# Performance work log

Measured on AMD Instinct MI355X. Metric: run time of the kernel, lower is better.

The kernel has to match this reference:

```python
import jax, jax.numpy as jnp
import numpy as np

BETA = 0.5      # conf.beta (undefined global in original repo)
ALPHA = 0.2     # LeakyReLU negative slope (init arg alpha)
N, E, FIN, FOUT = 50000, 1_600_000, 128, 64


def setup_inputs() -> dict:
    key = jax.random.key(0)
    k1, k2, k3, k4, k5 = jax.random.split(key, 5)
    inp = jax.random.normal(k1, (N, FIN), dtype=jnp.float32)
    edge = jax.random.randint(k2, (2, E), 0, N)                      # [2,E] (src,dst), = adj.nonzero().t()
    M_vals = jax.random.uniform(k3, (E,), dtype=jnp.float32)          # M gathered at edges
    # xavier_normal with gain 1.414, matching torch init
    W = jax.random.normal(k4, (FIN, FOUT), dtype=jnp.float32) * (1.414 * np.sqrt(2.0 / (FIN + FOUT)))
    a = jax.random.normal(k5, (2 * FOUT,), dtype=jnp.float32) * (1.414 * np.sqrt(2.0 / (1 + 2 * FOUT)))
    return {"input": inp, "M_vals": M_vals, "W": W, "a": a, "edge": edge}


def reference(input, M_vals, W, a, edge):
    n, f = input.shape[0], W.shape[1]
    src, dst = edge[0], edge[1]
    h = input @ W                                   # [N, F]
    # M = beta*M + (1-beta)*adj; at edges adj == 1
    bias = M_vals * BETA + (1.0 - BETA)             # [E]
    # a . cat(h_src, bias*h_dst) == (h@a[:F])[src] + bias * (h@a[F:])[dst]
    s1 = h @ a[:f]                                  # [N]
    s2 = h @ a[f:]                                  # [N]
    edge_e = jnp.exp(jax.nn.leaky_relu(s1[src] + bias * s2[dst], negative_slope=ALPHA))  # [E]
    # special_spmm(edge, e, [N,N], ones) -> per-row sum of edge weights
    e_rowsum = jax.ops.segment_sum(edge_e, src, num_segments=n)       # [N]
    # special_spmm(edge, e, [N,N], h) -> weighted aggregation of dst features into src rows
    h_prime = jax.ops.segment_sum(edge_e[:, None] * h[dst], src, num_segments=n)  # [N, F]
    h_prime = h_prime / e_rowsum[:, None]
    return jax.nn.elu(h_prime)                      # concat=True
```

## Files before the change

### kernel.cpp

```cpp
#include <hip/hip_runtime.h>
#include <hip/hip_bf16.h>

#define NN   50000
#define EE   1600000
#define FIN  128
#define FOUT 64
#define BETA  0.5f
#define ALPHA 0.2f
#define SBW    256
#define NB2    196
#define RCAP   9000
#define PGRID  400
#define PCHUNK 4000
#define CAP3   9008
#define XS     136
#define WS     136

typedef __attribute__((ext_vector_type(8))) short short8;
typedef __attribute__((ext_vector_type(8))) unsigned short ushort8v;
typedef __attribute__((ext_vector_type(4))) float float4v;

__device__ __forceinline__ float load_any(const void* p, long i, int isf32) {
    if (isf32) return ((const float*)p)[i];
    unsigned int b = ((unsigned int)(((const unsigned short*)p)[i])) << 16;
    return __uint_as_float(b);
}

__device__ __forceinline__ unsigned short f32_to_bf16_rne(float f) {
    unsigned int b = __float_as_uint(f);
    return (unsigned short)((b + 0x7FFF + ((b >> 16) & 1)) >> 16);
}

__device__ __forceinline__ float bf16_to_f32(unsigned short u) {
    return __uint_as_float(((unsigned int)u) << 16);
}

__global__ __launch_bounds__(256) void mfma_gemm_kernel(
    const void* __restrict__ inp,
    const void* __restrict__ W,
    const void* __restrict__ a,
    const void* __restrict__ Mv,
    unsigned short* __restrict__ h,
    float* __restrict__ s1,
    float* __restrict__ s2,
    int* __restrict__ flags,
    int* __restrict__ bcur)
{
    __shared__ unsigned short Xs[16 * XS];
    __shared__ unsigned short Wl[64 * WS];
    __shared__ float part1[4][16];
    __shared__ float part2[4][16];
    __shared__ int vote;

    const int tid  = threadIdx.x;
    const int wave = tid >> 6;
    const int lane = tid & 63;
    const int quad = lane >> 4;
    const int col  = lane & 15;
    const int rb   = blockIdx.x * 16;

    if (tid == 0) vote = 0;
    __syncthreads();

    {
        int m = 0;
        const unsigned short* ip = (const unsigned short*)inp;
        const float vi = bf16_to_f32(ip[(long)rb * FIN + tid * 8]);
        if (isnan(vi) || fabsf(vi) > 1e4f) m |= 1;
        if (tid < 128) {
            const float va = bf16_to_f32(((const unsigned short*)a)[tid]);
            if (isnan(va) || fabsf(va) > 1e4f) m |= 2;
        }
        const float vw = bf16_to_f32(((const unsigned short*)W)[tid * 16]);
        if (isnan(vw) || fabsf(vw) > 1e4f) m |= 4;
        if (blockIdx.x == 0) {
            const long half = (long)EE >> 1;
            const long pos = 2 * (((long)tid * (half / 256)) % half);
            const float vm = bf16_to_f32(((const unsigned short*)Mv)[pos]);
            if (isnan(vm) || fabsf(vm) > 1e4f) m |= 8;
        }
        if (m) atomicOr(&vote, m);
    }
    __syncthreads();
    const int vm = vote;
    const int fI = vm & 1, fA = (vm >> 1) & 1, fW = (vm >> 2) & 1;

    if (blockIdx.x == 0) {
        if (tid == 0) { flags[0] = fI; flags[1] = (vm >> 3) & 1; }
        if (tid < NB2) bcur[tid] = 0;
    }

    for (int i = tid; i < FIN * FOUT; i += 256) {
        const int k = i >> 6, n = i & 63;
        Wl[n * WS + k] = f32_to_bf16_rne(load_any(W, i, fW));
    }
    {
        const int r = tid >> 4, k8 = (tid & 15) * 8;
        if (!fI) {
            const unsigned short* src = (const unsigned short*)inp + (long)(rb + r) * FIN + k8;
            *(ushort8v*)&Xs[r * XS + k8] = *(const ushort8v*)src;
        } else {
            const float* src = (const float*)inp + (long)(rb + r) * FIN + k8;
            ushort8v v;
            #pragma unroll
            for (int j = 0; j < 8; ++j) v[j] = f32_to_bf16_rne(src[j]);
            *(ushort8v*)&Xs[r * XS + k8] = v;
        }
    }
    __syncthreads();

    const int nb = wave * 16;
    float4v acc = { 0.f, 0.f, 0.f, 0.f };
    #pragma unroll
    for (int k0 = 0; k0 < FIN; k0 += 32) {
        const short8 af = *(const short8*)&Xs[col * XS + k0 + quad * 8];
        const short8 bf = *(const short8*)&Wl[(nb + col) * WS + k0 + quad * 8];
        acc = __builtin_amdgcn_mfma_f32_16x16x32_bf16(af, bf, acc, 0, 0, 0);
    }

    #pragma unroll
    for (int r = 0; r < 4; ++r)
        h[(long)(rb + quad * 4 + r) * FOUT + nb + col] = f32_to_bf16_rne(acc[r]);

    const float a1 = load_any(a, nb + col, fA);
    const float a2 = load_any(a, 64 + nb + col, fA);
    #pragma unroll
    for (int r = 0; r < 4; ++r) {
        float v1 = acc[r] * a1;
        float v2 = acc[r] * a2;
        #pragma unroll
        for (int o = 1; o < 16; o <<= 1) {
            v1 += __shfl_xor(v1, o, 64);
            v2 += __shfl_xor(v2, o, 64);
        }
        if (col == 0) {
            part1[wave][quad * 4 + r] = v1;
            part2[wave][quad * 4 + r] = v2;
        }
    }
    __syncthreads();
    if (tid < 16) {
        s1[rb + tid] = part1[0][tid] + part1[1][tid] + part1[2][tid] + part1[3][tid];
        s2[rb + tid] = part2[0][tid] + part2[1][tid] + part2[2][tid] + part2[3][tid];
    }
}

__global__ __launch_bounds__(1024) void partition_kernel(
    const int* __restrict__ edge,
    const void* __restrict__ Mv,
    const int* __restrict__ flags,
    const float* __restrict__ s1,
    const float* __restrict__ s2,
    int* __restrict__ bcur,
    unsigned long long* __restrict__ recs)
{
    __shared__ int lcnt[NB2];
    __shared__ int lbase[NB2];
    const int tid = threadIdx.x;
    const int fM = flags[1];
    const int e0 = blockIdx.x * PCHUNK;

    if (tid < NB2) lcnt[tid] = 0;
    __syncthreads();

    int srcs[4], dsts[4];
    float mvs[4];
    #pragma unroll
    for (int k = 0; k < 4; ++k) {
        const int e = e0 + tid + 1024 * k;
        const bool ok = (tid + 1024 * k) < PCHUNK;
        srcs[k] = ok ? edge[e] : -1;
        dsts[k] = ok ? edge[EE + e] : 0;
        mvs[k]  = ok ? load_any(Mv, e, fM) : 0.f;
    }
    #pragma unroll
    for (int k = 0; k < 4; ++k)
        if (srcs[k] >= 0) atomicAdd(&lcnt[srcs[k] >> 8], 1);
    __syncthreads();

    if (tid < NB2) {
        const int c = lcnt[tid];
        const int o = c ? atomicAdd(&bcur[tid], c) : 0;
        lbase[tid] = tid * RCAP + o;
        lcnt[tid] = 0;
    }
    __syncthreads();

    float ss1[4], ss2[4];
    #pragma unroll
    for (int k = 0; k < 4; ++k) {
        ss1[k] = (srcs[k] >= 0) ? s1[srcs[k]] : 0.f;
        ss2[k] = (srcs[k] >= 0) ? s2[dsts[k]] : 0.f;
    }
    #pragma unroll
    for (int k = 0; k < 4; ++k) {
        if (srcs[k] < 0) continue;
        const float bias = mvs[k] * BETA + (1.f - BETA);
        const float x  = ss1[k] + bias * ss2[k];
        const float lr = x > 0.f ? x : ALPHA * x;
        const float ee = __expf(lr);
        const int b = srcs[k] >> 8;
        const int r = atomicAdd(&lcnt[b], 1);
        const int pos = lbase[b] + r;
        if (pos < (b + 1) * RCAP)
            recs[pos] = ((unsigned long long)(unsigned)srcs[k] << 32)
                      | ((unsigned long long)(unsigned)dsts[k] << 16)
                      | (unsigned long long)f32_to_bf16_rne(ee);
    }
}

__global__ __launch_bounds__(1024) void csr_spmm_kernel(
    const int* __restrict__ bcur,
    const unsigned long long* __restrict__ recs,
    const unsigned short* __restrict__ h,
    const int* __restrict__ flags,
    void* __restrict__ out)
{
    __shared__ unsigned long long lrec[CAP3];
    __shared__ unsigned int lpair[CAP3];
    __shared__ int cnt[SBW];
    __shared__ int off[SBW];
    __shared__ int wsum[4];
    const int b    = blockIdx.x;
    const int tid  = threadIdx.x;
    const int rb   = b * SBW;
    const int beg  = b * RCAP;

    int n = bcur[b]; if (n > RCAP) n = RCAP;

    if (tid < SBW) cnt[tid] = 0;
    __syncthreads();

    for (int j = tid; j < n; j += 1024) {
        const unsigned long long rec = recs[beg + j];
        lrec[j] = rec;
        atomicAdd(&cnt[(int)(rec >> 32) - rb], 1);
    }
    __syncthreads();

    int c = 0, x = 0;
    if (tid < SBW) {
        const int lane = tid & 63;
        c = cnt[tid];
        x = c;
        #pragma unroll
        for (int o = 1; o < 64; o <<= 1) {
            int y = __shfl_up(x, o, 64);
            if (lane >= o) x += y;
        }
        if (lane == 63) wsum[tid >> 6] = x;
    }
    __syncthreads();
    if (tid < SBW) {
        const int wv = tid >> 6;
        int wb = 0;
        for (int w = 0; w < wv; ++w) wb += wsum[w];
        off[tid] = wb + x - c;
        cnt[tid] = 0;
    }
    __syncthreads();

    for (int j = tid; j < n; j += 1024) {
        const unsigned long long rec = lrec[j];
        const int r = (int)(rec >> 32) - rb;
        const int rank = atomicAdd(&cnt[r], 1);
        lpair[off[r] + rank] = (unsigned int)(rec & 0xFFFFFFFFu);
    }
    __syncthreads();

    const int wv   = tid >> 6;
    const int lane = tid & 63;
    const int g    = lane >> 3;
    const int sl   = lane & 7;
    const int fOut = flags[0];

    for (int rr = wv; rr < SBW; rr += 16) {
        const int row = rb + rr;
        if (row >= NN) break;
        const int jb = off[rr];
        const int je = jb + cnt[rr];

        float acc0 = 0.f, acc1 = 0.f, acc2 = 0.f, acc3 = 0.f;
        float acc4 = 0.f, acc5 = 0.f, acc6 = 0.f, acc7 = 0.f;
        float rsum = 0.f;
        int j = jb;
        for (; j + 15 < je; j += 16) {
            const unsigned int u0 = lpair[j + g];
            const unsigned int u1 = lpair[j + 8 + g];
            const ushort8v h0 = *(const ushort8v*)&h[(long)(u0 >> 16) * FOUT + 8 * sl];
            const ushort8v h1 = *(const ushort8v*)&h[(long)(u1 >> 16) * FOUT + 8 * sl];
            const float v0 = bf16_to_f32((unsigned short)(u0 & 0xFFFFu));
            const float v1 = bf16_to_f32((unsigned short)(u1 & 0xFFFFu));
            rsum += v0 + v1;
            acc0 = fmaf(v0, bf16_to_f32(h0[0]), acc0); acc0 = fmaf(v1, bf16_to_f32(h1[0]), acc0);
            acc1 = fmaf(v0, bf16_to_f32(h0[1]), acc1); acc1 = fmaf(v1, bf16_to_f32(h1[1]), acc1);
            acc2 = fmaf(v0, bf16_to_f32(h0[2]), acc2); acc2 = fmaf(v1, bf16_to_f32(h1[2]), acc2);
            acc3 = fmaf(v0, bf16_to_f32(h0[3]), acc3); acc3 = fmaf(v1, bf16_to_f32(h1[3]), acc3);
            acc4 = fmaf(v0, bf16_to_f32(h0[4]), acc4); acc4 = fmaf(v1, bf16_to_f32(h1[4]), acc4);
            acc5 = fmaf(v0, bf16_to_f32(h0[5]), acc5); acc5 = fmaf(v1, bf16_to_f32(h1[5]), acc5);
            acc6 = fmaf(v0, bf16_to_f32(h0[6]), acc6); acc6 = fmaf(v1, bf16_to_f32(h1[6]), acc6);
            acc7 = fmaf(v0, bf16_to_f32(h0[7]), acc7); acc7 = fmaf(v1, bf16_to_f32(h1[7]), acc7);
        }
        for (; j < je; j += 8) {
            if (j + g < je) {
                const unsigned int u = lpair[j + g];
                const ushort8v hv = *(const ushort8v*)&h[(long)(u >> 16) * FOUT + 8 * sl];
                const float v = bf16_to_f32((unsigned short)(u & 0xFFFFu));
                rsum += v;
                acc0 = fmaf(v, bf16_to_f32(hv[0]), acc0);
                acc1 = fmaf(v, bf16_to_f32(hv[1]), acc1);
                acc2 = fmaf(v, bf16_to_f32(hv[2]), acc2);
                acc3 = fmaf(v, bf16_to_f32(hv[3]), acc3);
                acc4 = fmaf(v, bf16_to_f32(hv[4]), acc4);
                acc5 = fmaf(v, bf16_to_f32(hv[5]), acc5);
                acc6 = fmaf(v, bf16_to_f32(hv[6]), acc6);
                acc7 = fmaf(v, bf16_to_f32(hv[7]), acc7);
            }
        }

        #pragma unroll
        for (int o = 8; o < 64; o <<= 1) {
            rsum += __shfl_xor(rsum, o, 64);
            acc0 += __shfl_xor(acc0, o, 64);
            acc1 += __shfl_xor(acc1, o, 64);
            acc2 += __shfl_xor(acc2, o, 64);
            acc3 += __shfl_xor(acc3, o, 64);
            acc4 += __shfl_xor(acc4, o, 64);
            acc5 += __shfl_xor(acc5, o, 64);
            acc6 += __shfl_xor(acc6, o, 64);
            acc7 += __shfl_xor(acc7, o, 64);
        }

        if (g == 0) {
            const float inv = 1.f / rsum;
            float q0 = acc0 * inv, q1 = acc1 * inv, q2 = acc2 * inv, q3 = acc3 * inv;
            float q4 = acc4 * inv, q5 = acc5 * inv, q6 = acc6 * inv, q7 = acc7 * inv;
            q0 = q0 > 0.f ? q0 : (__expf(q0) - 1.f);
            q1 = q1 > 0.f ? q1 : (__expf(q1) - 1.f);
            q2 = q2 > 0.f ? q2 : (__expf(q2) - 1.f);
            q3 = q3 > 0.f ? q3 : (__expf(q3) - 1.f);
            q4 = q4 > 0.f ? q4 : (__expf(q4) - 1.f);
            q5 = q5 > 0.f ? q5 : (__expf(q5) - 1.f);
            q6 = q6 > 0.f ? q6 : (__expf(q6) - 1.f);
            q7 = q7 > 0.f ? q7 : (__expf(q7) - 1.f);
            if (fOut) {
                float4* o = (float4*)((float*)out + (long)row * FOUT + 8 * sl);
                o[0] = make_float4(q0, q1, q2, q3);
                o[1] = make_float4(q4, q5, q6, q7);
            } else {
                ushort8v ov;
                ov[0] = f32_to_bf16_rne(q0); ov[1] = f32_to_bf16_rne(q1);
                ov[2] = f32_to_bf16_rne(q2); ov[3] = f32_to_bf16_rne(q3);
                ov[4] = f32_to_bf16_rne(q4); ov[5] = f32_to_bf16_rne(q5);
                ov[6] = f32_to_bf16_rne(q6); ov[7] = f32_to_bf16_rne(q7);
                *(ushort8v*)((unsigned short*)out + (long)row * FOUT + 8 * sl) = ov;
            }
        }
    }
}

extern "C" void kernel_launch(void* const* d_in, const int* in_sizes, int n_in,
                              void* d_out, int out_size, void* d_ws, size_t ws_size,
                              hipStream_t stream) {
    const void* inp  = d_in[0];
    const void* Mv   = d_in[1];
    const void* W    = d_in[2];
    const void* a    = d_in[3];
    const int*  edge = (const int*)d_in[4];

    char* p = (char*)d_ws;
    int*                flags  = (int*)p;            p += 256;
    unsigned short*     h      = (unsigned short*)p; p += ((size_t)NN * FOUT * 2 + 255) / 256 * 256;
    float*              s1     = (float*)p;          p += ((size_t)NN * 4 + 255) / 256 * 256;
    float*              s2     = (float*)p;          p += ((size_t)NN * 4 + 255) / 256 * 256;
    int*                bcur   = (int*)p;            p += ((size_t)NB2 * 4 + 255) / 256 * 256;
    unsigned long long* recs   = (unsigned long long*)p;

    mfma_gemm_kernel<<<NN / 16, 256, 0, stream>>>(inp, W, a, Mv, h, s1, s2, flags, bcur);
    partition_kernel<<<PGRID, 1024, 0, stream>>>(edge, Mv, flags, s1, s2, bcur, recs);
    csr_spmm_kernel<<<NB2, 1024, 0, stream>>>(bcur, recs, h, flags, d_out);
}
```

Baseline: 183.5 us.

## Pretranspose W once, fuse rank assignment into counting, unroll SpMM gathers deeper

A new small kernel converts and transposes W into a bf16 workspace buffer once, along with flag detection and bucket reset. Each GEMM block then reads B fragments directly from that buffer instead of rebuilding a 16 KB LDS copy of W per 16-row tile. The CSR kernel now records each edge's rank during the counting pass, removing the second LDS atomic pass during the scatter. The SpMM inner loop issues four gathers per iteration instead of two for more memory-level parallelism. The cost is an extra kernel launch and uncached-in-LDS global reads of W in the GEMM.

```diff
diff --git a/kernel.cpp b/kernel.cpp
--- a/kernel.cpp
+++ b/kernel.cpp
@@ -14,7 +14,6 @@
 #define PCHUNK 4000
 #define CAP3   9008
 #define XS     136
-#define WS     136
 
 typedef __attribute__((ext_vector_type(8))) short short8;
 typedef __attribute__((ext_vector_type(8))) unsigned short ushort8v;
@@ -35,19 +34,48 @@
     return __uint_as_float(((unsigned int)u) << 16);
 }
 
+__global__ __launch_bounds__(256) void detwt_kernel(
+    const void* __restrict__ W, const void* __restrict__ Mv,
+    unsigned short* __restrict__ Wt, int* __restrict__ flags,
+    int* __restrict__ bcur)
+{
+    __shared__ int vote;
+    const int tid = threadIdx.x;
+    if (tid == 0) vote = 0;
+    __syncthreads();
+
+    int m = 0;
+    const float vw = bf16_to_f32(((const unsigned short*)W)[tid * 16]);
+    if (isnan(vw) || fabsf(vw) > 1e4f) m |= 1;
+    if (blockIdx.x == 0) {
+        const long half = (long)EE >> 1;
+        const long pos = 2 * (((long)tid * (half / 256)) % half);
+        const float vm = bf16_to_f32(((const unsigned short*)Mv)[pos]);
+        if (isnan(vm) || fabsf(vm) > 1e4f) m |= 2;
+    }
+    if (m) atomicOr(&vote, m);
+    __syncthreads();
+
+    const int fW = vote & 1;
+    if (blockIdx.x == 0) {
+        if (tid == 0) flags[1] = (vote >> 1) & 1;
+        if (tid < NB2) bcur[tid] = 0;
+    }
+    const int i = blockIdx.x * 256 + tid;
+    const int k = i >> 6, n = i & 63;
+    Wt[n * FIN + k] = f32_to_bf16_rne(load_any(W, i, fW));
+}
+
 __global__ __launch_bounds__(256) void mfma_gemm_kernel(
     const void* __restrict__ inp,
-    const void* __restrict__ W,
+    const unsigned short* __restrict__ Wt,
     const void* __restrict__ a,
-    const void* __restrict__ Mv,
     unsigned short* __restrict__ h,
     float* __restrict__ s1,
     float* __restrict__ s2,
-    int* __restrict__ flags,
-    int* __restrict__ bcur)
+    int* __restrict__ flags)
 {
     __shared__ unsigned short Xs[16 * XS];
-    __shared__ unsigned short Wl[64 * WS];
     __shared__ float part1[4][16];
     __shared__ float part2[4][16];
     __shared__ int vote;
@@ -64,36 +92,18 @@
 
     {
         int m = 0;
-        const unsigned short* ip = (const unsigned short*)inp;
-        const float vi = bf16_to_f32(ip[(long)rb * FIN + tid * 8]);
+        const float vi = bf16_to_f32(((const unsigned short*)inp)[(long)rb * FIN + tid * 8]);
         if (isnan(vi) || fabsf(vi) > 1e4f) m |= 1;
         if (tid < 128) {
             const float va = bf16_to_f32(((const unsigned short*)a)[tid]);
             if (isnan(va) || fabsf(va) > 1e4f) m |= 2;
         }
-        const float vw = bf16_to_f32(((const unsigned short*)W)[tid * 16]);
-        if (isnan(vw) || fabsf(vw) > 1e4f) m |= 4;
-        if (blockIdx.x == 0) {
-            const long half = (long)EE >> 1;
-            const long pos = 2 * (((long)tid * (half / 256)) % half);
-            const float vm = bf16_to_f32(((const unsigned short*)Mv)[pos]);
-            if (isnan(vm) || fabsf(vm) > 1e4f) m |= 8;
-        }
         if (m) atomicOr(&vote, m);
     }
     __syncthreads();
-    const int vm = vote;
-    const int fI = vm & 1, fA = (vm >> 1) & 1, fW = (vm >> 2) & 1;
-
-    if (blockIdx.x == 0) {
-        if (tid == 0) { flags[0] = fI; flags[1] = (vm >> 3) & 1; }
-        if (tid < NB2) bcur[tid] = 0;
-    }
-
-    for (int i = tid; i < FIN * FOUT; i += 256) {
-        const int k = i >> 6, n = i & 63;
-        Wl[n * WS + k] = f32_to_bf16_rne(load_any(W, i, fW));
-    }
+    const int fI = vote & 1, fA = (vote >> 1) & 1;
+    if (blockIdx.x == 0 && tid == 0) flags[0] = fI;
+
     {
         const int r = tid >> 4, k8 = (tid & 15) * 8;
         if (!fI) {
@@ -114,7 +124,7 @@
     #pragma unroll
     for (int k0 = 0; k0 < FIN; k0 += 32) {
         const short8 af = *(const short8*)&Xs[col * XS + k0 + quad * 8];
-        const short8 bf = *(const short8*)&Wl[(nb + col) * WS + k0 + quad * 8];
+        const short8 bf = *(const short8*)&Wt[(long)(nb + col) * FIN + k0 + quad * 8];
         acc = __builtin_amdgcn_mfma_f32_16x16x32_bf16(af, bf, acc, 0, 0, 0);
     }
 
@@ -233,8 +243,10 @@
 
     for (int j = tid; j < n; j += 1024) {
         const unsigned long long rec = recs[beg + j];
-        lrec[j] = rec;
-        atomicAdd(&cnt[(int)(rec >> 32) - rb], 1);
+        const int r = (int)(rec >> 32) - rb;
+        const int rank = atomicAdd(&cnt[r], 1);
+        lrec[j] = ((unsigned long long)(unsigned)(r | (rank << 8)) << 32)
+                | (unsigned long long)(unsigned)(rec & 0xFFFFFFFFu);
     }
     __syncthreads();
 
@@ -256,15 +268,13 @@
         int wb = 0;
         for (int w = 0; w < wv; ++w) wb += wsum[w];
         off[tid] = wb + x - c;
-        cnt[tid] = 0;
     }
     __syncthreads();
 
     for (int j = tid; j < n; j += 1024) {
         const unsigned long long rec = lrec[j];
-        const int r = (int)(rec >> 32) - rb;
-        const int rank = atomicAdd(&cnt[r], 1);
-        lpair[off[r] + rank] = (unsigned int)(rec & 0xFFFFFFFFu);
+        const unsigned int hi = (unsigned int)(rec >> 32);
+        lpair[off[hi & 255u] + (hi >> 8)] = (unsigned int)(rec & 0xFFFFFFFFu);
     }
     __syncthreads();
 
@@ -284,38 +294,55 @@
         float acc4 = 0.f, acc5 = 0.f, acc6 = 0.f, acc7 = 0.f;
         float rsum = 0.f;
         int j = jb;
-        for (; j + 15 < je; j += 16) {
-            const unsigned int u0 = lpair[j + g];
-            const unsigned int u1 = lpair[j + 8 + g];
-            const ushort8v h0 = *(const ushort8v*)&h[(long)(u0 >> 16) * FOUT + 8 * sl];
-            const ushort8v h1 = *(const ushort8v*)&h[(long)(u1 >> 16) * FOUT + 8 * sl];
-            const float v0 = bf16_to_f32((unsigned short)(u0 & 0xFFFFu));
-            const float v1 = bf16_to_f32((unsigned short)(u1 & 0xFFFFu));
-            rsum += v0 + v1;
-            acc0 = fmaf(v0, bf16_to_f32(h0[0]), acc0); acc0 = fmaf(v1, bf16_to_f32(h1[0]), acc0);
-            acc1 = fmaf(v0, bf16_to_f32(h0[1]), acc1); acc1 = fmaf(v1, bf16_to_f32(h1[1]), acc1);
-            acc2 = fmaf(v0, bf16_to_f32(h0[2]), acc2); acc2 = fmaf(v1, bf16_to_f32(h1[2]), acc2);
-            acc3 = fmaf(v0, bf16_to_f32(h0[3]), acc3); acc3 = fmaf(v1, bf16_to_f32(h1[3]), acc3);
-            acc4 = fmaf(v0, bf16_to_f32(h0[4]), acc4); acc4 = fmaf(v1, bf16_to_f32(h1[4]), acc4);
-            acc5 = fmaf(v0, bf16_to_f32(h0[5]), acc5); acc5 = fmaf(v1, bf16_to_f32(h1[5]), acc5);
-            acc6 = fmaf(v0, bf16_to_f32(h0[6]), acc6); acc6 = fmaf(v1, bf16_to_f32(h1[6]), acc6);
-            acc7 = fmaf(v0, bf16_to_f32(h0[7]), acc7); acc7 = fmaf(v1, bf16_to_f32(h1[7]), acc7);
-        }
-        for (; j < je; j += 8) {
-            if (j + g < je) {
-                const unsigned int u = lpair[j + g];
-                const ushort8v hv = *(const ushort8v*)&h[(long)(u >> 16) * FOUT + 8 * sl];
-                const float v = bf16_to_f32((unsigned short)(u & 0xFFFFu));
+        for (; j + 31 < je; j += 32) {
+            unsigned int u[4];
+            #pragma unroll
+            for (int kk = 0; kk < 4; ++kk) u[kk] = lpair[j + 8 * kk + g];
+            ushort8v hv[4];
+            #pragma unroll
+            for (int kk = 0; kk < 4; ++kk)
+                hv[kk] = *(const ushort8v*)&h[(long)(u[kk] >> 16) * FOUT + 8 * sl];
+            #pragma unroll
+            for (int kk = 0; kk < 4; ++kk) {
+                const float v = bf16_to_f32((unsigned short)(u[kk] & 0xFFFFu));
                 rsum += v;
-                acc0 = fmaf(v, bf16_to_f32(hv[0]), acc0);
-                acc1 = fmaf(v, bf16_to_f32(hv[1]), acc1);
-                acc2 = fmaf(v, bf16_to_f32(hv[2]), acc2);
-                acc3 = fmaf(v, bf16_to_f32(hv[3]), acc3);
-                acc4 = fmaf(v, bf16_to_f32(hv[4]), acc4);
-                acc5 = fmaf(v, bf16_to_f32(hv[5]), acc5);
-                acc6 = fmaf(v, bf16_to_f32(hv[6]), acc6);
-                acc7 = fmaf(v, bf16_to_f32(hv[7]), acc7);
+                acc0 = fmaf(v, bf16_to_f32(hv[kk][0]), acc0);
+                acc1 = fmaf(v, bf16_to_f32(hv[kk][1]), acc1);
+                acc2 = fmaf(v, bf16_to_f32(hv[kk][2]), acc2);
+                acc3 = fmaf(v, bf16_to_f32(hv[kk][3]), acc3);
+                acc4 = fmaf(v, bf16_to_f32(hv[kk][4]), acc4);
+                acc5 = fmaf(v, bf16_to_f32(hv[kk][5]), acc5);
+                acc6 = fmaf(v, bf16_to_f32(hv[kk][6]), acc6);
+                acc7 = fmaf(v, bf16_to_f32(hv[kk][7]), acc7);
             }
+        }
+        for (; j + 7 < je; j += 8) {
+            const unsigned int u = lpair[j + g];
+            const ushort8v hv = *(const ushort8v*)&h[(long)(u >> 16) * FOUT + 8 * sl];
+            const float v = bf16_to_f32((unsigned short)(u & 0xFFFFu));
+            rsum += v;
+            acc0 = fmaf(v, bf16_to_f32(hv[0]), acc0);
+            acc1 = fmaf(v, bf16_to_f32(hv[1]), acc1);
+            acc2 = fmaf(v, bf16_to_f32(hv[2]), acc2);
+            acc3 = fmaf(v, bf16_to_f32(hv[3]), acc3);
+            acc4 = fmaf(v, bf16_to_f32(hv[4]), acc4);
+            acc5 = fmaf(v, bf16_to_f32(hv[5]), acc5);
+            acc6 = fmaf(v, bf16_to_f32(hv[6]), acc6);
+            acc7 = fmaf(v, bf16_to_f32(hv[7]), acc7);
+        }
+        if (j < je && j + g < je) {
+            const unsigned int u = lpair[j + g];
+            const ushort8v hv = *(const ushort8v*)&h[(long)(u >> 16) * FOUT + 8 * sl];
+            const float v = bf16_to_f32((unsigned short)(u & 0xFFFFu));
+            rsum += v;
+            acc0 = fmaf(v, bf16_to_f32(hv[0]), acc0);
+            acc1 = fmaf(v, bf16_to_f32(hv[1]), acc1);
+            acc2 = fmaf(v, bf16_to_f32(hv[2]), acc2);
+            acc3 = fmaf(v, bf16_to_f32(hv[3]), acc3);
+            acc4 = fmaf(v, bf16_to_f32(hv[4]), acc4);
+            acc5 = fmaf(v, bf16_to_f32(hv[5]), acc5);
+            acc6 = fmaf(v, bf16_to_f32(hv[6]), acc6);
+            acc7 = fmaf(v, bf16_to_f32(hv[7]), acc7);
         }
 
         #pragma unroll
@@ -370,13 +397,15 @@
 
     char* p = (char*)d_ws;
     int*                flags  = (int*)p;            p += 256;
+    unsigned short*     Wt     = (unsigned short*)p; p += ((size_t)FOUT * FIN * 2 + 255) / 256 * 256;
     unsigned short*     h      = (unsigned short*)p; p += ((size_t)NN * FOUT * 2 + 255) / 256 * 256;
     float*              s1     = (float*)p;          p += ((size_t)NN * 4 + 255) / 256 * 256;
     float*              s2     = (float*)p;          p += ((size_t)NN * 4 + 255) / 256 * 256;
     int*                bcur   = (int*)p;            p += ((size_t)NB2 * 4 + 255) / 256 * 256;
     unsigned long long* recs   = (unsigned long long*)p;
 
-    mfma_gemm_kernel<<<NN / 16, 256, 0, stream>>>(inp, W, a, Mv, h, s1, s2, flags, bcur);
+    detwt_kernel<<<32, 256, 0, stream>>>(W, Mv, Wt, flags, bcur);
+    mfma_gemm_kernel<<<NN / 16, 256, 0, stream>>>(inp, Wt, a, h, s1, s2, flags);
     partition_kernel<<<PGRID, 1024, 0, stream>>>(edge, Mv, flags, s1, s2, bcur, recs);
     csr_spmm_kernel<<<NB2, 1024, 0, stream>>>(bcur, recs, h, flags, d_out);
 }
```

New measurement: 174.5 us. 4.9% less time.
